# Kernel optimization log

Hardware: AMD Instinct MI355X
Metric: run time of the kernel (lower is better)

The kernel has to match this reference:

```python
import jax, jax.numpy as jnp
import numpy as np

B, LQ, LK, D = 4, 2048, 2048, 512
EPS = 1e-8  # torch cosine_similarity eps


def setup_inputs() -> dict:
    key = jax.random.key(0)
    ks = jax.random.split(key, 8)
    s = 1.0 / np.sqrt(D)
    return {
        "query": jax.random.normal(ks[0], (B, LQ, D), jnp.float32),
        "key": jax.random.normal(ks[1], (B, LK, D), jnp.float32),
        "value": jax.random.normal(ks[2], (B, LK, D), jnp.float32),
        "Wq": jax.random.normal(ks[3], (D, D), jnp.float32) * s,
        "bq": jax.random.normal(ks[4], (D,), jnp.float32) * s,
        "Wk": jax.random.normal(ks[5], (D, D), jnp.float32) * s,
        "bk": jax.random.normal(ks[6], (D,), jnp.float32) * s,
        "scoring_weights": jnp.ones((3,), jnp.float32) / 3.0,
    }


def reference(query, key, value, Wq, bq, Wk, bk, scoring_weights):
    # fused tanh-QK transforms (torch Linear: x @ W.T + b)
    q = jnp.tanh(jnp.einsum('bqd,ed->bqe', query, Wq) + bq)  # [B,LQ,D]
    k = jnp.tanh(jnp.einsum('bkd,ed->bke', key, Wk) + bk)    # [B,LK,D]

    dot = jnp.einsum('bqd,bkd->bqk', q, k)                   # [B,LQ,LK]
    qn = jnp.linalg.norm(q, axis=-1)                         # [B,LQ]
    kn = jnp.linalg.norm(k, axis=-1)                         # [B,LK]
    # cosine_similarity: dot / max(|q|*|k|, eps)
    cos = dot / jnp.maximum(qn[:, :, None] * kn[:, None, :], EPS)
    # -cdist (p=2): sqrt(|q|^2 + |k|^2 - 2 q.k), clamped at 0
    sq = jnp.maximum(qn[:, :, None] ** 2 + kn[:, None, :] ** 2 - 2.0 * dot, 0.0)
    euc = -jnp.sqrt(sq)

    w = jax.nn.softmax(scoring_weights)
    scores = w[0] * dot + w[1] * cos + w[2] * euc
    attn = jax.nn.softmax(scores, axis=-1)                   # [B,LQ,LK]
    context = jnp.einsum('bqk,bkd->bqd', attn, value)        # [B,LQ,D]
    return context, attn
```

## Files before the change

kernel.cpp:

```cpp
#include <hip/hip_runtime.h>
#include <cstdint>
#include <cstddef>

namespace {

constexpr int BATCH = 4;
constexpr int LQ = 2048;
constexpr int LK = 2048;
constexpr int D = 512;
constexpr int MQ = BATCH * LQ;

using f16 = _Float16;
typedef _Float16 f16x8 __attribute__((ext_vector_type(8)));
typedef _Float16 f16x4 __attribute__((ext_vector_type(4)));
typedef float f32x4 __attribute__((ext_vector_type(4)));

__device__ __forceinline__ f16x8 cvt8(const float4 a, const float4 b) {
  f16x8 h;
  h[0] = (f16)a.x; h[1] = (f16)a.y; h[2] = (f16)a.z; h[3] = (f16)a.w;
  h[4] = (f16)b.x; h[5] = (f16)b.y; h[6] = (f16)b.z; h[7] = (f16)b.w;
  return h;
}

typedef __attribute__((address_space(1))) const void gas_void;
typedef __attribute__((address_space(3))) void las_void;
__device__ __forceinline__ void gload_lds16(const void* g, void* l) {
  __builtin_amdgcn_global_load_lds((gas_void*)g, (las_void*)l, 16, 0, 0);
}

__global__ __launch_bounds__(256) void prep_kernel(
    const float* __restrict__ query, const float* __restrict__ keyp,
    const float* __restrict__ value, const float* __restrict__ Wq,
    const float* __restrict__ Wk, const float* __restrict__ bq,
    const float* __restrict__ bk, f16* __restrict__ qh, f16* __restrict__ kh,
    float* __restrict__ qnsqp, float* __restrict__ knsqp,
    f16* __restrict__ vt) {
  __shared__ __align__(16) char smem[21504];
  const int bid0 = blockIdx.x;
  const int t = threadIdx.x;

  if (bid0 >= 512) {
    const int bid = bid0 - 512;
    const int kt = bid & 31;
    const int dt = (bid >> 5) & 7;
    const int b = bid >> 8;
    const int k0 = kt * 64, d0 = dt * 64;
    f16(*T)[72] = reinterpret_cast<f16(*)[72]>(smem);
#pragma unroll
    for (int i = 0; i < 4; ++i) {
      const int u = t + i * 256;
      const int k = u >> 4;
      const int d4 = (u & 15) << 2;
      float4 x = *reinterpret_cast<const float4*>(
          value + (size_t)(b * LK + k0 + k) * D + d0 + d4);
      T[d4 + 0][k] = (f16)x.x;
      T[d4 + 1][k] = (f16)x.y;
      T[d4 + 2][k] = (f16)x.z;
      T[d4 + 3][k] = (f16)x.w;
    }
    __syncthreads();
#pragma unroll
    for (int i = 0; i < 2; ++i) {
      const int u = t + i * 256;
      const int d = u >> 3;
      const int k8 = (u & 7) << 3;
      f16x8 h = *reinterpret_cast<const f16x8*>(&T[d][k8]);
      *reinterpret_cast<f16x8*>(vt + (size_t)(b * D + d0 + d) * LK + k0 + k8) =
          h;
    }
    return;
  }

  const int which = bid0 >> 8;
  const float* __restrict__ X = which ? keyp : query;
  const float* __restrict__ W = which ? Wk : Wq;
  const float* __restrict__ bias = which ? bk : bq;
  f16* __restrict__ out = which ? kh : qh;
  float* __restrict__ nsqp = which ? knsqp : qnsqp;

  const int bid = bid0 & 255;
  const int tm = bid & 63;
  const int tn = bid >> 6;
  const int brow = tm * 128, bcol = tn * 128;
  const int lane = t & 63;
  const int wid = t >> 6;
  const int wr = (wid >> 1) * 64, wc = (wid & 1) * 64;
  const int lr = lane & 15;
  const int lk = (lane >> 4) << 3;
  const int g4 = (lane >> 4) << 2;

  f16(*As)[40] = reinterpret_cast<f16(*)[40]>(smem);
  f16(*Bs)[40] = reinterpret_cast<f16(*)[40]>(smem + 10240);
  float(*s_ss)[2] = reinterpret_cast<float(*)[2]>(smem + 20480);

  f32x4 acc[4][4] = {};

  for (int k0 = 0; k0 < D; k0 += 32) {
#pragma unroll
    for (int i = 0; i < 2; ++i) {
      const int u = t + i * 256;
      const int r = u >> 2;
      const int c8 = (u & 3) << 3;
      const float4* pa =
          reinterpret_cast<const float4*>(X + (size_t)(brow + r) * D + k0 + c8);
      *reinterpret_cast<f16x8*>(&As[r][c8]) = cvt8(pa[0], pa[1]);
      const float4* pb =
          reinterpret_cast<const float4*>(W + (size_t)(bcol + r) * D + k0 + c8);
      *reinterpret_cast<f16x8*>(&Bs[r][c8]) = cvt8(pb[0], pb[1]);
    }
    __syncthreads();
    f16x8 af[4], bf[4];
#pragma unroll
    for (int m = 0; m < 4; ++m)
      af[m] = *reinterpret_cast<const f16x8*>(&As[wr + m * 16 + lr][lk]);
#pragma unroll
    for (int n = 0; n < 4; ++n)
      bf[n] = *reinterpret_cast<const f16x8*>(&Bs[wc + n * 16 + lr][lk]);
#pragma unroll
    for (int m = 0; m < 4; ++m)
#pragma unroll
      for (int n = 0; n < 4; ++n)
        acc[m][n] =
            __builtin_amdgcn_mfma_f32_16x16x32_f16(bf[n], af[m], acc[m][n], 0, 0, 0);
    __syncthreads();
  }

  float4 bv[4];
#pragma unroll
  for (int n = 0; n < 4; ++n)
    bv[n] = *reinterpret_cast<const float4*>(&bias[bcol + wc + n * 16 + g4]);

#pragma unroll
  for (int m = 0; m < 4; ++m) {
    const int row = brow + wr + m * 16 + lr;
    float ss = 0.f;
#pragma unroll
    for (int n = 0; n < 4; ++n) {
      float th[4];
#pragma unroll
      for (int r = 0; r < 4; ++r) {
        th[r] = tanhf(acc[m][n][r] + ((const float*)&bv[n])[r]);
        ss = fmaf(th[r], th[r], ss);
      }
      f16x4 h4;
      h4[0] = (f16)th[0]; h4[1] = (f16)th[1];
      h4[2] = (f16)th[2]; h4[3] = (f16)th[3];
      *reinterpret_cast<f16x4*>(out + (size_t)row * D + bcol + wc + n * 16 + g4) =
          h4;
    }
    ss += __shfl_xor(ss, 16);
    ss += __shfl_xor(ss, 32);
    if (lane < 16) s_ss[wr + m * 16 + lr][wid & 1] = ss;
  }
  __syncthreads();
  if (t < 128) nsqp[(size_t)(brow + t) * 4 + tn] = s_ss[t][0] + s_ss[t][1];
}

template <bool RAW16>
__global__ __launch_bounds__(256, 4) void scores_kernel(
    const f16* __restrict__ qh, const f16* __restrict__ kh,
    const float* __restrict__ qnsqp, const float* __restrict__ knsqp,
    const float* __restrict__ sw, float* __restrict__ attn,
    f16* __restrict__ sraw, float2* __restrict__ tstats) {
  const int bid0 = blockIdx.x;
  const int bid = (bid0 & 7) * 128 + (bid0 >> 3);
  const int tn = bid & 15;
  const int tm = (bid >> 4) & 15;
  const int b = bid >> 8;
  const int brow = tm * 128, bcol = tn * 128;
  const int t = threadIdx.x;
  const int lane = t & 63;
  const int wid = t >> 6;
  const int wr = (wid >> 1) * 64, wc = (wid & 1) * 64;
  const int lr = lane & 15;
  const int lk = (lane >> 4) << 3;
  const int g4 = (lane >> 4) << 2;

  __shared__ f16 As[128 * 64];
  __shared__ f16 Bs[128 * 64];
  __shared__ float s_m[128][2];
  __shared__ float s_l[128][2];

  f32x4 acc[4][4] = {};

  const int srow = lane >> 3;
  const int scol = ((lane & 7) ^ srow) << 4;
  const char* aBase = (const char*)(qh + (size_t)(b * LQ + brow) * D);
  const char* bBase = (const char*)(kh + (size_t)(b * LK + bcol) * D);
  const int swz = (lr & 7) << 4;

  for (int k0 = 0; k0 < D; k0 += 64) {
#pragma unroll
    for (int i = 0; i < 4; ++i) {
      const int chunk = wid * 4 + i;
      const int row = chunk * 8 + srow;
      gload_lds16(aBase + (size_t)row * (D * 2) + k0 * 2 + scol,
                  (char*)As + chunk * 1024);
      gload_lds16(bBase + (size_t)row * (D * 2) + k0 * 2 + scol,
                  (char*)Bs + chunk * 1024);
    }
    __syncthreads();
    f16x8 af[2][4], bf[2][4];
#pragma unroll
    for (int h = 0; h < 2; ++h) {
      const int cb = h * 64 + lk * 2;
#pragma unroll
      for (int m = 0; m < 4; ++m)
        af[h][m] = *(const f16x8*)((const char*)As + (wr + m * 16 + lr) * 128 +
                                   (cb ^ swz));
#pragma unroll
      for (int n = 0; n < 4; ++n)
        bf[h][n] = *(const f16x8*)((const char*)Bs + (wc + n * 16 + lr) * 128 +
                                   (cb ^ swz));
    }
#pragma unroll
    for (int h = 0; h < 2; ++h)
#pragma unroll
      for (int m = 0; m < 4; ++m)
#pragma unroll
        for (int n = 0; n < 4; ++n)
          acc[m][n] = __builtin_amdgcn_mfma_f32_16x16x32_f16(bf[h][n], af[h][m],
                                                             acc[m][n], 0, 0, 0);
    __syncthreads();
  }

  const float s0 = sw[0], s1 = sw[1], s2 = sw[2];
  const float smx = fmaxf(s0, fmaxf(s1, s2));
  float w0 = __expf(s0 - smx), w1 = __expf(s1 - smx), w2 = __expf(s2 - smx);
  const float winv = 1.f / (w0 + w1 + w2);
  w0 *= winv; w1 *= winv; w2 *= winv;

  float qn2_[4], w1rq[4];
#pragma unroll
  for (int m = 0; m < 4; ++m) {
    const float4 qp = *reinterpret_cast<const float4*>(
        &qnsqp[(size_t)(b * LQ + brow + wr + m * 16 + lr) * 4]);
    const float v = (qp.x + qp.y) + (qp.z + qp.w);
    qn2_[m] = v;
    w1rq[m] = w1 * rsqrtf(fmaxf(v, 1e-16f));
  }
  float kn2[4][4], rk[4][4];
#pragma unroll
  for (int n = 0; n < 4; ++n) {
#pragma unroll
    for (int r = 0; r < 4; ++r) {
      const int col = bcol + wc + n * 16 + g4 + r;
      const float4 kp = *reinterpret_cast<const float4*>(
          &knsqp[(size_t)(b * LK + col) * 4]);
      const float v = (kp.x + kp.y) + (kp.z + kp.w);
      kn2[n][r] = v;
      rk[n][r] = rsqrtf(fmaxf(v, 1e-16f));
    }
  }

#pragma unroll
  for (int m = 0; m < 4; ++m) {
    const int rl = wr + m * 16 + lr;
    const int row = brow + rl;
    float mx = -3.4e38f;
#pragma unroll
    for (int n = 0; n < 4; ++n) {
      float4 o;
#pragma unroll
      for (int r = 0; r < 4; ++r) {
        const float dot = acc[m][n][r];
        const float qk2 = qn2_[m] + kn2[n][r];
        const float st = sqrtf(fmaxf(qk2 - 2.f * dot, 0.f));
        const float c = fmaf(w1rq[m], rk[n][r], w0);
        const float s = fmaf(dot, c, -w2 * st);
        ((float*)&o)[r] = s;
        acc[m][n][r] = s;
        mx = fmaxf(mx, s);
      }
      if constexpr (!RAW16) {
        *reinterpret_cast<float4*>(attn + (size_t)(b * LQ + row) * LK + bcol +
                                   wc + n * 16 + g4) = o;
      }
    }
    mx = fmaxf(mx, __shfl_xor(mx, 16));
    mx = fmaxf(mx, __shfl_xor(mx, 32));
    if (lane < 16) s_m[rl][wid & 1] = mx;
  }
  __syncthreads();

#pragma unroll
  for (int m = 0; m < 4; ++m) {
    const int rl = wr + m * 16 + lr;
    const int row = brow + rl;
    const float Mt = fmaxf(s_m[rl][0], s_m[rl][1]);
    float es = 0.f;
#pragma unroll
    for (int n = 0; n < 4; ++n) {
      float e0 = __expf(acc[m][n][0] - Mt);
      float e1 = __expf(acc[m][n][1] - Mt);
      float e2 = __expf(acc[m][n][2] - Mt);
      float e3 = __expf(acc[m][n][3] - Mt);
      es += (e0 + e1) + (e2 + e3);
      if constexpr (RAW16) {
        f16x4 h4;
        h4[0] = (f16)e0; h4[1] = (f16)e1; h4[2] = (f16)e2; h4[3] = (f16)e3;
        *reinterpret_cast<f16x4*>(sraw + (size_t)(b * LQ + row) * LK + bcol +
                                  wc + n * 16 + g4) = h4;
      }
    }
    es += __shfl_xor(es, 16);
    es += __shfl_xor(es, 32);
    if (lane < 16) s_l[rl][wid & 1] = es;
  }
  __syncthreads();
  if (t < 128) {
    tstats[(size_t)(b * LQ + brow + t) * 16 + tn] =
        make_float2(fmaxf(s_m[t][0], s_m[t][1]), s_l[t][0] + s_l[t][1]);
  }
}

__global__ __launch_bounds__(256) void normalize_kernel(
    float* __restrict__ attn, const float2* __restrict__ tstats) {
  const int row = blockIdx.x;
  const int t = threadIdx.x;
  __shared__ float sM, sI;
  if (t < 16) {
    float2 st = tstats[(size_t)row * 16 + t];
    float M = st.x;
    M = fmaxf(M, __shfl_xor(M, 8));
    M = fmaxf(M, __shfl_xor(M, 4));
    M = fmaxf(M, __shfl_xor(M, 2));
    M = fmaxf(M, __shfl_xor(M, 1));
    float l = st.y * __expf(st.x - M);
    l += __shfl_xor(l, 8);
    l += __shfl_xor(l, 4);
    l += __shfl_xor(l, 2);
    l += __shfl_xor(l, 1);
    if (t == 0) { sM = M; sI = 1.f / l; }
  }
  __syncthreads();
  const float M = sM, invL = sI;
  float* rp = attn + (size_t)row * LK + t * 8;
  float4 v0 = *reinterpret_cast<const float4*>(rp);
  float4 v1 = *reinterpret_cast<const float4*>(rp + 4);
  v0.x = __expf(v0.x - M) * invL; v0.y = __expf(v0.y - M) * invL;
  v0.z = __expf(v0.z - M) * invL; v0.w = __expf(v0.w - M) * invL;
  v1.x = __expf(v1.x - M) * invL; v1.y = __expf(v1.y - M) * invL;
  v1.z = __expf(v1.z - M) * invL; v1.w = __expf(v1.w - M) * invL;
  *reinterpret_cast<float4*>(rp) = v0;
  *reinterpret_cast<float4*>(rp + 4) = v1;
}

template <bool NORM>
__global__ __launch_bounds__(512, 4) void pv_kernel(
    float* __restrict__ attnf, const f16* __restrict__ sraw,
    const f16* __restrict__ vt, const float2* __restrict__ tstats,
    float* __restrict__ ctx) {
  const int bid0 = blockIdx.x;
  const int bid = (bid0 & 7) * 64 + (bid0 >> 3);
  const int tn = bid & 3;
  const int tm = (bid >> 2) & 31;
  const int b = bid >> 7;
  const int brow = tm * 64, bcol = tn * 128;
  const int t = threadIdx.x;
  const int lane = t & 63;
  const int wid = t >> 6;
  const int wr = (wid >> 1) * 16, wc = (wid & 1) * 64;
  const int lr = lane & 15;
  const int lk = (lane >> 4) << 3;
  const int g4 = (lane >> 4) << 2;

  __shared__ f16 As[64 * 64];
  __shared__ f16 Bs[128 * 64];
  __shared__ float sScale[64][17];

  f32x4 acc[4] = {};

  const int srow = lane >> 3;
  const int scol = ((lane & 7) ^ srow) << 4;
  const size_t arow0 = (size_t)(b * LQ + brow);
  const char* bBase = (const char*)(vt + (size_t)(b * D + bcol) * LK);
  const int swz = (lr & 7) << 4;

  const int arow = t >> 3;
  const int c16 = (t & 7) << 4;
  const int csrc = c16 ^ ((arow & 7) << 4);
  const char* aRow =
      (const char*)sraw + (arow0 + arow) * (size_t)LK * 2 + csrc;

  if constexpr (NORM) {
    if (t < 256) {
      const int prow = t >> 2;
      const int j4 = (t & 3) * 4;
      const float4* tp =
          reinterpret_cast<const float4*>(&tstats[(arow0 + prow) * 16 + j4]);
      const float4 a = tp[0], c = tp[1];
      float m_ = fmaxf(fmaxf(a.x, a.z), fmaxf(c.x, c.z));
      m_ = fmaxf(m_, __shfl_xor(m_, 1));
      m_ = fmaxf(m_, __shfl_xor(m_, 2));
      float l_ = a.y * __expf(a.x - m_) + a.w * __expf(a.z - m_) +
                 c.y * __expf(c.x - m_) + c.w * __expf(c.z - m_);
      l_ += __shfl_xor(l_, 1);
      l_ += __shfl_xor(l_, 2);
      const float invL = 1.f / l_;
      sScale[prow][j4 + 0] = __expf(a.x - m_) * invL;
      sScale[prow][j4 + 1] = __expf(a.z - m_) * invL;
      sScale[prow][j4 + 2] = __expf(c.x - m_) * invL;
      sScale[prow][j4 + 3] = __expf(c.z - m_) * invL;
    }
    __syncthreads();
  }

  f16x8 hcur;
  if constexpr (NORM) hcur = *(const f16x8*)(aRow);

  for (int k0 = 0; k0 < LK; k0 += 64) {
#pragma unroll
    for (int i = 0; i < 2; ++i) {
      const int chunk = wid * 2 + i;
      const int row = chunk * 8 + srow;
      gload_lds16(bBase + (size_t)row * (LK * 2) + k0 * 2 + scol,
                  (char*)Bs + chunk * 1024);
    }
    if constexpr (NORM) {
      f16x8 hnext;
      if (k0 + 64 < LK) hnext = *(const f16x8*)(aRow + (k0 + 64) * 2);
      const float sc = sScale[arow][k0 >> 7];
      const f16 sch = (f16)sc;
      const f16x8 scv = {sch, sch, sch, sch, sch, sch, sch, sch};
      const f16x8 hv = hcur * scv;
      *(f16x8*)((char*)As + arow * 128 + c16) = hv;
      if ((k0 >> 9) == tn) {
        float4 e0, e1;
        e0.x = (float)hv[0]; e0.y = (float)hv[1];
        e0.z = (float)hv[2]; e0.w = (float)hv[3];
        e1.x = (float)hv[4]; e1.y = (float)hv[5];
        e1.z = (float)hv[6]; e1.w = (float)hv[7];
        float* op = attnf + (arow0 + arow) * LK + k0 + (csrc >> 1);
        *reinterpret_cast<float4*>(op) = e0;
        *reinterpret_cast<float4*>(op + 4) = e1;
      }
      hcur = hnext;
    } else {
      const float4* ps = (const float4*)((const char*)attnf +
                                         ((arow0 + arow) * LK + k0) * 4 +
                                         csrc * 2);
      *(f16x8*)((char*)As + arow * 128 + c16) = cvt8(ps[0], ps[1]);
    }
    __syncthreads();
    f16x8 af[2], bf[2][4];
#pragma unroll
    for (int h = 0; h < 2; ++h) {
      const int cb = h * 64 + lk * 2;
      af[h] = *(const f16x8*)((const char*)As + (wr + lr) * 128 + (cb ^ swz));
#pragma unroll
      for (int n = 0; n < 4; ++n)
        bf[h][n] = *(const f16x8*)((const char*)Bs + (wc + n * 16 + lr) * 128 +
                                   (cb ^ swz));
    }
#pragma unroll
    for (int h = 0; h < 2; ++h)
#pragma unroll
      for (int n = 0; n < 4; ++n)
        acc[n] = __builtin_amdgcn_mfma_f32_16x16x32_f16(bf[h][n], af[h],
                                                        acc[n], 0, 0, 0);
    __syncthreads();
  }

  const int row = brow + wr + lr;
  float* rowp = ctx + (size_t)(b * LQ + row) * D + bcol + wc;
#pragma unroll
  for (int n = 0; n < 4; ++n) {
    float4 o;
    o.x = acc[n][0]; o.y = acc[n][1];
    o.z = acc[n][2]; o.w = acc[n][3];
    *reinterpret_cast<float4*>(rowp + n * 16 + g4) = o;
  }
}

}

extern "C" void kernel_launch(void* const* d_in, const int* in_sizes, int n_in,
                              void* d_out, int out_size, void* d_ws,
                              size_t ws_size, hipStream_t stream) {
  const float* query = (const float*)d_in[0];
  const float* key = (const float*)d_in[1];
  const float* value = (const float*)d_in[2];
  const float* Wq = (const float*)d_in[3];
  const float* bq = (const float*)d_in[4];
  const float* Wk = (const float*)d_in[5];
  const float* bk = (const float*)d_in[6];
  const float* sw = (const float*)d_in[7];

  float* ctx = (float*)d_out;
  float* attn = (float*)d_out + (size_t)BATCH * LQ * D;

  char* ws = (char*)d_ws;
  f16* vt = (f16*)ws;
  f16* qh = (f16*)(ws + (size_t)(8u << 20));
  f16* kh = (f16*)(ws + (size_t)(16u << 20));
  float* qnsqp = (float*)(ws + (size_t)(24u << 20));
  float* knsqp = qnsqp + (size_t)MQ * 4;
  float2* tstats = (float2*)(ws + (size_t)(25u << 20));
  f16* sraw = (f16*)(ws + (size_t)(26u << 20));
  const size_t ws_needed =
      ((size_t)(26u << 20)) + (size_t)BATCH * LQ * LK * sizeof(f16);
  const bool useA16 = ws_size >= ws_needed;

  prep_kernel<<<1536, 256, 0, stream>>>(query, key, value, Wq, Wk, bq, bk, qh,
                                        kh, qnsqp, knsqp, vt);
  if (useA16) {
    scores_kernel<true><<<1024, 256, 0, stream>>>(qh, kh, qnsqp, knsqp, sw,
                                                  attn, sraw, tstats);
    pv_kernel<true><<<512, 512, 0, stream>>>(attn, sraw, vt, tstats, ctx);
  } else {
    scores_kernel<false><<<1024, 256, 0, stream>>>(qh, kh, qnsqp, knsqp, sw,
                                                   attn, sraw, tstats);
    normalize_kernel<<<MQ, 256, 0, stream>>>(attn, tstats);
    pv_kernel<false><<<512, 512, 0, stream>>>(attn, sraw, vt, tstats, ctx);
  }
}
```

Before: 101.9 us.

## Double-buffer LDS tiles in PV kernel to overlap loads with MFMA

```diff
diff --git a/kernel.cpp b/kernel.cpp
--- a/kernel.cpp
+++ b/kernel.cpp
@@ -365,9 +365,9 @@
   const int lk = (lane >> 4) << 3;
   const int g4 = (lane >> 4) << 2;
 
-  __shared__ f16 As[64 * 64];
-  __shared__ f16 Bs[128 * 64];
-  __shared__ float sScale[64][17];
+  __shared__ f16 As[2][64 * 64];
+  __shared__ f16 Bs[2][128 * 64];
+  __shared__ f16 sScale[64][17];
 
   f32x4 acc[4] = {};
 
@@ -398,60 +398,82 @@
       l_ += __shfl_xor(l_, 1);
       l_ += __shfl_xor(l_, 2);
       const float invL = 1.f / l_;
-      sScale[prow][j4 + 0] = __expf(a.x - m_) * invL;
-      sScale[prow][j4 + 1] = __expf(a.z - m_) * invL;
-      sScale[prow][j4 + 2] = __expf(c.x - m_) * invL;
-      sScale[prow][j4 + 3] = __expf(c.z - m_) * invL;
-    }
-    __syncthreads();
-  }
-
-  f16x8 hcur;
-  if constexpr (NORM) hcur = *(const f16x8*)(aRow);
-
+      sScale[prow][j4 + 0] = (f16)(__expf(a.x - m_) * invL);
+      sScale[prow][j4 + 1] = (f16)(__expf(a.z - m_) * invL);
+      sScale[prow][j4 + 2] = (f16)(__expf(c.x - m_) * invL);
+      sScale[prow][j4 + 3] = (f16)(__expf(c.z - m_) * invL);
+    }
+    __syncthreads();
+  }
+
+#define PV_STAGE_B(bufi, kk)                                                 \
+  _Pragma("unroll") for (int i_ = 0; i_ < 2; ++i_) {                         \
+    const int chunk_ = wid * 2 + i_;                                         \
+    const int row_ = chunk_ * 8 + srow;                                      \
+    gload_lds16(bBase + (size_t)row_ * (LK * 2) + (kk)*2 + scol,             \
+                (char*)Bs[bufi] + chunk_ * 1024);                            \
+  }
+
+#define PV_STAGE_A_NORM(bufi, kk, hreg)                                      \
+  {                                                                          \
+    const f16 sch_ = sScale[arow][(kk) >> 7];                                \
+    const f16x8 scv_ = {sch_, sch_, sch_, sch_, sch_, sch_, sch_, sch_};     \
+    const f16x8 hv_ = (hreg)*scv_;                                           \
+    *(f16x8*)((char*)As[bufi] + arow * 128 + c16) = hv_;                     \
+    if (((kk) >> 9) == tn) {                                                 \
+      float4 e0_, e1_;                                                       \
+      e0_.x = (float)hv_[0]; e0_.y = (float)hv_[1];                          \
+      e0_.z = (float)hv_[2]; e0_.w = (float)hv_[3];                          \
+      e1_.x = (float)hv_[4]; e1_.y = (float)hv_[5];                          \
+      e1_.z = (float)hv_[6]; e1_.w = (float)hv_[7];                          \
+      float* op_ = attnf + (arow0 + arow) * LK + (kk) + (csrc >> 1);         \
+      *reinterpret_cast<float4*>(op_) = e0_;                                 \
+      *reinterpret_cast<float4*>(op_ + 4) = e1_;                             \
+    }                                                                        \
+  }
+
+#define PV_STAGE_A_F32(bufi, kk)                                             \
+  {                                                                          \
+    const float4* ps_ = (const float4*)((const char*)attnf +                 \
+                                        ((arow0 + arow) * LK + (kk)) * 4 +   \
+                                        csrc * 2);                           \
+    *(f16x8*)((char*)As[bufi] + arow * 128 + c16) = cvt8(ps_[0], ps_[1]);    \
+  }
+
+  f16x8 hnext;
+  if constexpr (NORM) {
+    f16x8 h0 = *(const f16x8*)(aRow);
+    PV_STAGE_B(0, 0);
+    PV_STAGE_A_NORM(0, 0, h0);
+    hnext = *(const f16x8*)(aRow + 64 * 2);
+  } else {
+    PV_STAGE_B(0, 0);
+    PV_STAGE_A_F32(0, 0);
+  }
+  __syncthreads();
+
+  int cur = 0;
   for (int k0 = 0; k0 < LK; k0 += 64) {
-#pragma unroll
-    for (int i = 0; i < 2; ++i) {
-      const int chunk = wid * 2 + i;
-      const int row = chunk * 8 + srow;
-      gload_lds16(bBase + (size_t)row * (LK * 2) + k0 * 2 + scol,
-                  (char*)Bs + chunk * 1024);
-    }
-    if constexpr (NORM) {
-      f16x8 hnext;
-      if (k0 + 64 < LK) hnext = *(const f16x8*)(aRow + (k0 + 64) * 2);
-      const float sc = sScale[arow][k0 >> 7];
-      const f16 sch = (f16)sc;
-      const f16x8 scv = {sch, sch, sch, sch, sch, sch, sch, sch};
-      const f16x8 hv = hcur * scv;
-      *(f16x8*)((char*)As + arow * 128 + c16) = hv;
-      if ((k0 >> 9) == tn) {
-        float4 e0, e1;
-        e0.x = (float)hv[0]; e0.y = (float)hv[1];
-        e0.z = (float)hv[2]; e0.w = (float)hv[3];
-        e1.x = (float)hv[4]; e1.y = (float)hv[5];
-        e1.z = (float)hv[6]; e1.w = (float)hv[7];
-        float* op = attnf + (arow0 + arow) * LK + k0 + (csrc >> 1);
-        *reinterpret_cast<float4*>(op) = e0;
-        *reinterpret_cast<float4*>(op + 4) = e1;
+    const int kn = k0 + 64;
+    if (kn < LK) {
+      PV_STAGE_B(cur ^ 1, kn);
+      if constexpr (NORM) {
+        PV_STAGE_A_NORM(cur ^ 1, kn, hnext);
+        if (kn + 64 < LK) hnext = *(const f16x8*)(aRow + (kn + 64) * 2);
+      } else {
+        PV_STAGE_A_F32(cur ^ 1, kn);
       }
-      hcur = hnext;
-    } else {
-      const float4* ps = (const float4*)((const char*)attnf +
-                                         ((arow0 + arow) * LK + k0) * 4 +
-                                         csrc * 2);
-      *(f16x8*)((char*)As + arow * 128 + c16) = cvt8(ps[0], ps[1]);
-    }
-    __syncthreads();
+    }
     f16x8 af[2], bf[2][4];
 #pragma unroll
     for (int h = 0; h < 2; ++h) {
       const int cb = h * 64 + lk * 2;
-      af[h] = *(const f16x8*)((const char*)As + (wr + lr) * 128 + (cb ^ swz));
+      af[h] =
+          *(const f16x8*)((const char*)As[cur] + (wr + lr) * 128 + (cb ^ swz));
 #pragma unroll
       for (int n = 0; n < 4; ++n)
-        bf[h][n] = *(const f16x8*)((const char*)Bs + (wc + n * 16 + lr) * 128 +
-                                   (cb ^ swz));
+        bf[h][n] = *(const f16x8*)((const char*)Bs[cur] +
+                                   (wc + n * 16 + lr) * 128 + (cb ^ swz));
     }
 #pragma unroll
     for (int h = 0; h < 2; ++h)
@@ -460,7 +482,11 @@
         acc[n] = __builtin_amdgcn_mfma_f32_16x16x32_f16(bf[h][n], af[h],
                                                         acc[n], 0, 0, 0);
     __syncthreads();
-  }
+    cur ^= 1;
+  }
+#undef PV_STAGE_B
+#undef PV_STAGE_A_NORM
+#undef PV_STAGE_A_F32
 
   const int row = brow + wr + lr;
   float* rowp = ctx + (size_t)(b * LQ + row) * D + bcol + wc;
```

Result: no change. 102.6 us (+0.7%).
